# Kernel optimization log

Hardware: AMD Instinct MI355X
Metric: run time of the kernel (lower is better)

## Reference

```python
import jax, jax.numpy as jnp
import numpy as np

N_IN = 1000000   # non-empty input octants at depth d
N_OUT = 125000   # parent octants at depth d-1 (stride-2 downsample)
C_IN = 96
C_OUT = 192
K = 8            # 2x2x2 kernel -> 8 children per parent
BN_EPS = 1e-5


def setup_inputs() -> dict:
    key = jax.random.key(0)
    k1, k2, k3, k4 = jax.random.split(key, 4)
    data = jax.random.normal(k1, (N_IN, C_IN), dtype=jnp.float32)
    # child-neighbor table: index into input rows; <0 would mean empty child
    neigh = jax.random.randint(k2, (N_OUT, K), 0, N_IN, dtype=jnp.int64)
    # OctreeConv weights [K, Cin, Cout] + bias, BatchNorm affine params
    fan_in = K * C_IN
    weights = jax.random.normal(k3, (K, C_IN, C_OUT), dtype=jnp.float32) / np.sqrt(fan_in)
    bias = jax.random.normal(k4, (C_OUT,), dtype=jnp.float32) * 0.01
    gamma = jnp.ones((C_OUT,), dtype=jnp.float32)
    beta = jnp.zeros((C_OUT,), dtype=jnp.float32)
    return {"data": data, "weights": weights, "bias": bias,
            "gamma": gamma, "beta": beta, "neigh": neigh}


def reference(data, weights, bias, gamma, beta, neigh):
    # --- OctreeConv, kernel 2x2x2, stride 2, nempty=True ---
    valid = neigh >= 0                                   # [M, K]
    idx = jnp.clip(neigh, 0)                             # safe gather index
    gathered = data[idx]                                 # [M, K, Cin]
    gathered = jnp.where(valid[:, :, None], gathered, 0.0)
    out = jnp.einsum('mkc,kcd->md', gathered, weights) + bias  # [M, Cout]
    # --- BatchNorm1d over node dim (training-mode batch stats) ---
    mean = jnp.mean(out, axis=0)
    var = jnp.var(out, axis=0)                           # biased variance
    out = (out - mean) * jax.lax.rsqrt(var + BN_EPS) * gamma + beta
    return out
```

## Files before the change

### kernel.cpp

```cpp
#include <hip/hip_runtime.h>

#define M_OUT   125000
#define CIN     96
#define COUT    192
#define KOCT    8
#define MT      128
#define LDB     104
#define BN_EPS  1e-5f

#define WS_WT_BYTE   4096

typedef __attribute__((ext_vector_type(8))) short bf16x8;
typedef __attribute__((ext_vector_type(4))) float f32x4;

__device__ __forceinline__ unsigned short f2bf(float f) {
    unsigned int u = __float_as_uint(f);
    u += 0x7FFF + ((u >> 16) & 1);
    return (unsigned short)(u >> 16);
}

__device__ __forceinline__ unsigned int pack2(float a, float b) {
    unsigned int ua = __float_as_uint(a);
    unsigned int ub = __float_as_uint(b);
    ua += 0x7FFF + ((ua >> 16) & 1);
    ub += 0x7FFF + ((ub >> 16) & 1);
    return (ua >> 16) | (ub & 0xFFFF0000u);
}

__device__ __forceinline__ bf16x8 pack8(const float4 h0, const float4 h1) {
    union { unsigned int u[4]; bf16x8 v; } r;
    r.u[0] = pack2(h0.x, h0.y);
    r.u[1] = pack2(h0.z, h0.w);
    r.u[2] = pack2(h1.x, h1.y);
    r.u[3] = pack2(h1.z, h1.w);
    return r.v;
}

__device__ __forceinline__ int sel8(const int4 a, const int4 b, int k) {
    switch (k & 7) {
        case 0: return a.x; case 1: return a.y; case 2: return a.z; case 3: return a.w;
        case 4: return b.x; case 5: return b.y; case 6: return b.z; default: return b.w;
    }
}

__global__ void prep_kernel(const float* __restrict__ W, float* __restrict__ ws_f,
                            unsigned short* __restrict__ wt) {
    int gid = blockIdx.x * blockDim.x + threadIdx.x;
    if (gid < 384) ws_f[gid] = 0.0f;
    if (gid < KOCT * COUT * LDB) {
        int c = gid % LDB;
        int rest = gid / LDB;
        int n = rest % COUT;
        int k = rest / COUT;
        float v = (c < CIN) ? W[(k * CIN + c) * COUT + n] : 0.0f;
        wt[gid] = f2bf(v);
    }
}

__global__ __launch_bounds__(512, 2)
void conv_kernel(const float* __restrict__ data,
                 const int* __restrict__ neigh,
                 const float* __restrict__ bias,
                 const unsigned short* __restrict__ wt,
                 float* __restrict__ out,
                 float* __restrict__ gsum) {
    __shared__ float stats[2 * COUT];

    const int t    = threadIdx.x;
    const int wave = t >> 6;
    const int lane = t & 63;
    const int quad = lane >> 4;
    const int l15  = lane & 15;
    const int rg   = wave >> 1;
    const int ch   = wave & 1;
    const int m0   = blockIdx.x * MT;
    const int row0 = m0 + rg * 32;

    for (int i = t; i < 2 * COUT; i += 512) stats[i] = 0.0f;
    __syncthreads();

    int4 nid[2][2];
#pragma unroll
    for (int rt = 0; rt < 2; ++rt) {
        int gm = row0 + rt * 16 + l15;
        if (gm < M_OUT) {
            nid[rt][0] = *reinterpret_cast<const int4*>(neigh + (size_t)gm * 8);
            nid[rt][1] = *reinterpret_cast<const int4*>(neigh + (size_t)gm * 8 + 4);
        } else {
            nid[rt][0] = make_int4(-1, -1, -1, -1);
            nid[rt][1] = make_int4(-1, -1, -1, -1);
        }
    }

    f32x4 acc[2][6];
    const f32x4 vz = {0.f, 0.f, 0.f, 0.f};
#pragma unroll
    for (int i = 0; i < 2; ++i)
#pragma unroll
        for (int j = 0; j < 6; ++j) acc[i][j] = vz;

    float4 arA[12], arB[12];
    bf16x8 af[2][3];

    auto gather = [&](float4 (&AR)[12], int K) {
#pragma unroll
        for (int rt = 0; rt < 2; ++rt) {
            int idx = sel8(nid[rt][0], nid[rt][1], K);
            const float* p = data + (size_t)idx * CIN + quad * 8;
#pragma unroll
            for (int ks = 0; ks < 3; ++ks)
#pragma unroll
                for (int h = 0; h < 2; ++h) {
                    float4 v = {0.f, 0.f, 0.f, 0.f};
                    if (idx >= 0) v = *reinterpret_cast<const float4*>(p + ks * 32 + h * 4);
                    AR[(rt * 3 + ks) * 2 + h] = v;
                }
        }
    };
    auto packA = [&](float4 (&AR)[12]) {
#pragma unroll
        for (int rt = 0; rt < 2; ++rt)
#pragma unroll
            for (int ks = 0; ks < 3; ++ks)
                af[rt][ks] = pack8(AR[(rt * 3 + ks) * 2], AR[(rt * 3 + ks) * 2 + 1]);
    };
    auto loadB = [&](bf16x8 (&BF)[6], int K, int KS) {
#pragma unroll
        for (int c = 0; c < 6; ++c) {
            int n = ch * 96 + c * 16 + l15;
            BF[c] = *reinterpret_cast<const bf16x8*>(
                wt + ((size_t)K * COUT + n) * LDB + KS * 32 + quad * 8);
        }
    };
    auto mfmaG = [&](bf16x8 (&BF)[6], int KS) {
#pragma unroll
        for (int rt = 0; rt < 2; ++rt)
#pragma unroll
            for (int c = 0; c < 6; ++c)
                acc[rt][c] = __builtin_amdgcn_mfma_f32_16x16x32_bf16(
                    af[rt][KS], BF[c], acc[rt][c], 0, 0, 0);
    };

    gather(arA, 0);
    gather(arB, 1);

    bf16x8 b0[6], b1[6];
#pragma unroll
    for (int k = 0; k < KOCT; ++k) {
        loadB(b0, k, 0);
        if (k & 1) packA(arB); else packA(arA);
        if (k < KOCT - 2) {
            if (k & 1) gather(arB, k + 2); else gather(arA, k + 2);
        }
        loadB(b1, k, 1);
        __builtin_amdgcn_sched_barrier(0);
        mfmaG(b0, 0);
        loadB(b0, k, 2);
        mfmaG(b1, 1);
        mfmaG(b0, 2);
    }

#pragma unroll
    for (int ct = 0; ct < 6; ++ct) {
        int col = ch * 96 + ct * 16 + l15;
        float b = bias[col];
        float s1 = 0.f, s2 = 0.f;
#pragma unroll
        for (int rt = 0; rt < 2; ++rt) {
#pragma unroll
            for (int r = 0; r < 4; ++r) {
                int gm = row0 + rt * 16 + quad * 4 + r;
                if (gm < M_OUT) {
                    float v = acc[rt][ct][r] + b;
                    out[(size_t)gm * COUT + col] = v;
                    s1 += v;
                    s2 += v * v;
                }
            }
        }
        s1 += __shfl_xor(s1, 16); s2 += __shfl_xor(s2, 16);
        s1 += __shfl_xor(s1, 32); s2 += __shfl_xor(s2, 32);
        if (quad == 0) {
            atomicAdd(&stats[col], s1);
            atomicAdd(&stats[COUT + col], s2);
        }
    }
    __syncthreads();
    for (int i = t; i < COUT; i += 512) {
        atomicAdd(&gsum[i], stats[i]);
        atomicAdd(&gsum[COUT + i], stats[COUT + i]);
    }
}

__global__ void norm_kernel(float* __restrict__ out,
                            const float* __restrict__ gsum,
                            const float* __restrict__ gamma,
                            const float* __restrict__ beta) {
    __shared__ float s_scale[COUT], s_shift[COUT];
    for (int i = threadIdx.x; i < COUT; i += blockDim.x) {
        const float inv_m = 1.0f / (float)M_OUT;
        float mean = gsum[i] * inv_m;
        float var  = gsum[COUT + i] * inv_m - mean * mean;
        float sc   = gamma[i] * rsqrtf(var + BN_EPS);
        s_scale[i] = sc;
        s_shift[i] = beta[i] - mean * sc;
    }
    __syncthreads();
    const int total4 = M_OUT * COUT / 4;
    int stride = gridDim.x * blockDim.x;
    for (int i = blockIdx.x * blockDim.x + threadIdx.x; i < total4; i += stride) {
        float4 v = reinterpret_cast<float4*>(out)[i];
        int c4 = (i % (COUT / 4)) * 4;
        v.x = v.x * s_scale[c4 + 0] + s_shift[c4 + 0];
        v.y = v.y * s_scale[c4 + 1] + s_shift[c4 + 1];
        v.z = v.z * s_scale[c4 + 2] + s_shift[c4 + 2];
        v.w = v.w * s_scale[c4 + 3] + s_shift[c4 + 3];
        reinterpret_cast<float4*>(out)[i] = v;
    }
}

extern "C" void kernel_launch(void* const* d_in, const int* in_sizes, int n_in,
                              void* d_out, int out_size, void* d_ws, size_t ws_size,
                              hipStream_t stream) {
    const float* data  = (const float*)d_in[0];
    const float* W     = (const float*)d_in[1];
    const float* bias  = (const float*)d_in[2];
    const float* gamma = (const float*)d_in[3];
    const float* beta  = (const float*)d_in[4];
    const int*   neigh = (const int*)d_in[5];
    float* out  = (float*)d_out;
    float* ws_f = (float*)d_ws;
    unsigned short* wt = (unsigned short*)((char*)d_ws + WS_WT_BYTE);

    prep_kernel<<<(KOCT * COUT * LDB + 255) / 256, 256, 0, stream>>>(W, ws_f, wt);

    int grid1 = (M_OUT + MT - 1) / MT;
    conv_kernel<<<grid1, 512, 0, stream>>>(data, neigh, bias, wt, out, ws_f);

    norm_kernel<<<4096, 256, 0, stream>>>(out, ws_f, gamma, beta);
}
```

Measured before the change: 720.3 us.

## Stage gathered input rows into swizzled LDS triple buffer via global_load_lds

```diff
diff --git a/kernel.cpp b/kernel.cpp
--- a/kernel.cpp
+++ b/kernel.cpp
@@ -64,6 +64,8 @@
                  const unsigned short* __restrict__ wt,
                  float* __restrict__ out,
                  float* __restrict__ gsum) {
+    __shared__ __align__(16) float Abuf[3][MT * CIN];
+    __shared__ int   idxs[MT * KOCT];
     __shared__ float stats[2 * COUT];
 
     const int t    = threadIdx.x;
@@ -76,8 +78,15 @@
     const int m0   = blockIdx.x * MT;
     const int row0 = m0 + rg * 32;
 
+    if (t < 256) {
+        int row = t >> 1, half = t & 1;
+        int gm = m0 + row;
+        int4 v = make_int4(0, 0, 0, 0);
+        if (gm < M_OUT) v = *reinterpret_cast<const int4*>(neigh + (size_t)gm * 8 + half * 4);
+        v.x = max(v.x, 0); v.y = max(v.y, 0); v.z = max(v.z, 0); v.w = max(v.w, 0);
+        *reinterpret_cast<int4*>(idxs + row * 8 + half * 4) = v;
+    }
     for (int i = t; i < 2 * COUT; i += 512) stats[i] = 0.0f;
-    __syncthreads();
 
     int4 nid[2][2];
 #pragma unroll
@@ -92,6 +101,31 @@
         }
     }
 
+    __syncthreads();
+
+    int srow[6], scol[6];
+#pragma unroll
+    for (int i = 0; i < 6; ++i) {
+        int off  = i * 8192 + t * 16;
+        int row  = off / 384;
+        int colb = off - row * 384;
+        srow[i] = row;
+        scol[i] = colb ^ ((row & 7) << 4);
+    }
+
+    auto stage = [&](int k2, int buf) {
+        char* dst = (char*)&Abuf[buf][0];
+#pragma unroll
+        for (int i = 0; i < 6; ++i) {
+            int idx = idxs[srow[i] * 8 + k2];
+            const char* src = (const char*)data + (size_t)idx * 384 + scol[i];
+            __builtin_amdgcn_global_load_lds(
+                (const __attribute__((address_space(1))) unsigned int*)src,
+                (__attribute__((address_space(3))) unsigned int*)(dst + i * 8192 + t * 16),
+                16, 0, 0);
+        }
+    };
+
     f32x4 acc[2][6];
     const f32x4 vz = {0.f, 0.f, 0.f, 0.f};
 #pragma unroll
@@ -99,65 +133,59 @@
 #pragma unroll
         for (int j = 0; j < 6; ++j) acc[i][j] = vz;
 
-    float4 arA[12], arB[12];
-    bf16x8 af[2][3];
-
-    auto gather = [&](float4 (&AR)[12], int K) {
+    const bf16x8 zfrag = {0, 0, 0, 0, 0, 0, 0, 0};
+
+    stage(0, 0);
+    asm volatile("s_waitcnt vmcnt(0)" ::: "memory");
+    stage(1, 1);
+
+#pragma unroll 1
+    for (int k = 0; k < KOCT; ++k) {
+        bf16x8 bq[3][6];
+        bf16x8 af[2][3];
+#pragma unroll
+        for (int ks = 0; ks < 3; ++ks)
+#pragma unroll
+            for (int c = 0; c < 6; ++c) {
+                int n = ch * 96 + c * 16 + l15;
+                bq[ks][c] = *reinterpret_cast<const bf16x8*>(
+                    wt + ((size_t)k * COUT + n) * LDB + ks * 32 + quad * 8);
+            }
+        __builtin_amdgcn_sched_barrier(0);
+        if (k < KOCT - 2) stage(k + 2, (k + 2) % 3);
+        __builtin_amdgcn_sched_barrier(0);
+        __builtin_amdgcn_s_barrier();
+        __builtin_amdgcn_sched_barrier(0);
+
+        const char* abase = (const char*)&Abuf[k % 3][0];
 #pragma unroll
         for (int rt = 0; rt < 2; ++rt) {
-            int idx = sel8(nid[rt][0], nid[rt][1], K);
-            const float* p = data + (size_t)idx * CIN + quad * 8;
-#pragma unroll
-            for (int ks = 0; ks < 3; ++ks)
-#pragma unroll
-                for (int h = 0; h < 2; ++h) {
-                    float4 v = {0.f, 0.f, 0.f, 0.f};
-                    if (idx >= 0) v = *reinterpret_cast<const float4*>(p + ks * 32 + h * 4);
-                    AR[(rt * 3 + ks) * 2 + h] = v;
-                }
-        }
-    };
-    auto packA = [&](float4 (&AR)[12]) {
-#pragma unroll
-        for (int rt = 0; rt < 2; ++rt)
-#pragma unroll
-            for (int ks = 0; ks < 3; ++ks)
-                af[rt][ks] = pack8(AR[(rt * 3 + ks) * 2], AR[(rt * 3 + ks) * 2 + 1]);
-    };
-    auto loadB = [&](bf16x8 (&BF)[6], int K, int KS) {
-#pragma unroll
-        for (int c = 0; c < 6; ++c) {
-            int n = ch * 96 + c * 16 + l15;
-            BF[c] = *reinterpret_cast<const bf16x8*>(
-                wt + ((size_t)K * COUT + n) * LDB + KS * 32 + quad * 8);
-        }
-    };
-    auto mfmaG = [&](bf16x8 (&BF)[6], int KS) {
-#pragma unroll
-        for (int rt = 0; rt < 2; ++rt)
-#pragma unroll
-            for (int c = 0; c < 6; ++c)
-                acc[rt][c] = __builtin_amdgcn_mfma_f32_16x16x32_bf16(
-                    af[rt][KS], BF[c], acc[rt][c], 0, 0, 0);
-    };
-
-    gather(arA, 0);
-    gather(arB, 1);
-
-    bf16x8 b0[6], b1[6];
-#pragma unroll
-    for (int k = 0; k < KOCT; ++k) {
-        loadB(b0, k, 0);
-        if (k & 1) packA(arB); else packA(arA);
-        if (k < KOCT - 2) {
-            if (k & 1) gather(arB, k + 2); else gather(arA, k + 2);
-        }
-        loadB(b1, k, 1);
-        __builtin_amdgcn_sched_barrier(0);
-        mfmaG(b0, 0);
-        loadB(b0, k, 2);
-        mfmaG(b1, 1);
-        mfmaG(b0, 2);
+            int row   = rg * 32 + rt * 16 + l15;
+            int rbase = row * 384;
+            int sw    = (row & 7) << 4;
+#pragma unroll
+            for (int ks = 0; ks < 3; ++ks) {
+                int c0 = ks * 128 + quad * 32;
+                float4 v0 = *reinterpret_cast<const float4*>(abase + rbase + (c0 ^ sw));
+                float4 v1 = *reinterpret_cast<const float4*>(abase + rbase + ((c0 + 16) ^ sw));
+                af[rt][ks] = pack8(v0, v1);
+            }
+            int idxr = sel8(nid[rt][0], nid[rt][1], k);
+            if (idxr < 0) { af[rt][0] = zfrag; af[rt][1] = zfrag; af[rt][2] = zfrag; }
+        }
+#pragma unroll
+        for (int ks = 0; ks < 3; ++ks)
+#pragma unroll
+            for (int rt = 0; rt < 2; ++rt)
+#pragma unroll
+                for (int c = 0; c < 6; ++c)
+                    acc[rt][c] = __builtin_amdgcn_mfma_f32_16x16x32_bf16(
+                        af[rt][ks], bq[ks][c], acc[rt][c], 0, 0, 0);
+
+        asm volatile("s_waitcnt lgkmcnt(0)" ::: "memory");
+        __builtin_amdgcn_sched_barrier(0);
+        __builtin_amdgcn_s_barrier();
+        __builtin_amdgcn_sched_barrier(0);
     }
 
 #pragma unroll
```

Result: faster. 644.2 us (-10.6%).
